# Kernel tuning notes

Hardware: AMD Instinct MI355X
Metric: run time of the kernel (lower is better)

## Reference

```python
import jax, jax.numpy as jnp
import numpy as np

N = 50000          # nodes
E = 600000         # edges
IN, H, HID = 3, 128, 64   # input_size, embed_size, decoder hidden
L = 5              # block_number (GRU layers)
EPS = 1e-12


def _l2norm(v):
    # F.normalize(v, p=2, dim=1)
    return v / jnp.maximum(jnp.linalg.norm(v, axis=1, keepdims=True), EPS)


def setup_inputs() -> dict:
    key = jax.random.key(0)
    ks = jax.random.split(key, 12)
    s = 0.05
    x = jax.random.normal(ks[0], (N, IN), dtype=jnp.float32)
    edge_idx = jax.random.randint(ks[1], (2, E), 0, N, dtype=jnp.int64)
    return {
        "x": x,
        "edge_idx": edge_idx,
        # encoder embed: Linear(IN, H)
        "W_embed": jax.random.normal(ks[2], (H, IN), dtype=jnp.float32) * s,
        "b_embed": jnp.zeros((H,), dtype=jnp.float32),
        # L stacked GRU(H, H) params, torch gate order (r, z, n)
        "w_ih": jax.random.normal(ks[3], (L, 3 * H, H), dtype=jnp.float32) * s,
        "w_hh": jax.random.normal(ks[4], (L, 3 * H, H), dtype=jnp.float32) * s,
        "b_ih": jax.random.normal(ks[5], (L, 3 * H), dtype=jnp.float32) * s,
        "b_hh": jax.random.normal(ks[6], (L, 3 * H), dtype=jnp.float32) * s,
        # decoder: Linear(H, HID) -> ReLU -> Linear(HID, 1)
        "W_hid": jax.random.normal(ks[7], (HID, H), dtype=jnp.float32) * s,
        "b_hid": jnp.zeros((HID,), dtype=jnp.float32),
        "W_out": jax.random.normal(ks[8], (1, HID), dtype=jnp.float32) * s,
        "b_out": jnp.zeros((1,), dtype=jnp.float32),
    }


def reference(x, edge_idx, W_embed, b_embed, w_ih, w_hh, b_ih, b_hh,
              W_hid, b_hid, W_out, b_out):
    row, col = edge_idx[0], edge_idx[1]
    n = x.shape[0]

    # symmetric degree normalization (deg + 1)^-0.5, identical every layer
    deg = jnp.zeros((n,), dtype=x.dtype).at[col].add(1.0) + 1.0
    dinv = deg ** -0.5
    norm = dinv[row] * dinv[col]            # [E]

    h0 = _l2norm(jax.nn.relu(x @ W_embed.T + b_embed))  # [N, H]

    def step(h, params):
        wih, whh, bih, bhh = params
        # message + add-aggregate: out[col] += norm * h[row]
        msg = norm[:, None] * h[row]                     # [E, H]
        agg = jax.ops.segment_sum(msg, col, num_segments=n)  # [N, H]
        # GRU step: input = agg, hidden = h (torch gate order r, z, n)
        gi = agg @ wih.T + bih                           # [N, 3H]
        gh = h @ whh.T + bhh                             # [N, 3H]
        i_r, i_z, i_n = jnp.split(gi, 3, axis=1)
        h_r, h_z, h_n = jnp.split(gh, 3, axis=1)
        r = jax.nn.sigmoid(i_r + h_r)
        zg = jax.nn.sigmoid(i_z + h_z)
        ng = jnp.tanh(i_n + r * h_n)
        hn = _l2norm((1.0 - zg) * ng + zg * h)
        return hn, hn

    _, hs = jax.lax.scan(step, h0, (w_ih, w_hh, b_ih, b_hh))  # hs: [L, N, H]
    all_h = jnp.concatenate([h0[None], hs], axis=0)           # [L+1, N, H]
    z = jnp.max(all_h, axis=0)                                # layer-wise max-pool

    z = jax.nn.relu(z @ W_hid.T + b_hid)
    return z @ W_out.T + b_out                                # [N, 1]
```

## Files before the change

### kernel.cpp

```cpp
#include <hip/hip_runtime.h>
#include <math.h>


#define NTHREADS 256
#define SCAN_CHUNK 1024

typedef __attribute__((ext_vector_type(8))) short s16x8;
typedef __attribute__((ext_vector_type(4))) float f32x4;

union U8 { s16x8 v; ushort4 h[2]; int4 q; };

__device__ __forceinline__ unsigned short f2bf(float f) {
  union { float f; unsigned u; } x; x.f = f;
  unsigned u = x.u + 0x7FFFu + ((x.u >> 16) & 1u);
  return (unsigned short)(u >> 16);
}
__device__ __forceinline__ float bf2f(unsigned short s) {
  union { unsigned u; float f; } x; x.u = ((unsigned)s) << 16;
  return x.f;
}
__device__ __forceinline__ float fast_sigmoid(float x) {
  return __builtin_amdgcn_rcpf(1.f + __expf(-x));
}
__device__ __forceinline__ float fast_tanh(float x) {
  return 1.f - 2.f * __builtin_amdgcn_rcpf(1.f + __expf(2.f * x));
}


__global__ void count_deg(const int* __restrict__ col, int* deg, int E) {
  int e = blockIdx.x * NTHREADS + threadIdx.x;
  if (e < E) atomicAdd(&deg[col[e]], 1);
}

__global__ void block_reduce(const int* __restrict__ cnt, int* __restrict__ bsum,
                             float* __restrict__ dinv, float* __restrict__ rdinv, int n) {
  __shared__ int red[NTHREADS];
  int b = blockIdx.x, t = threadIdx.x;
  int base = b * SCAN_CHUNK + t * 4;
  int s = 0;
#pragma unroll
  for (int i = 0; i < 4; ++i) {
    int idx = base + i;
    if (idx < n) {
      int c = cnt[idx];
      s += c;
      dinv[idx] = rsqrtf((float)c + 1.0f);
      rdinv[idx] = sqrtf((float)c + 1.0f);
    }
  }
  red[t] = s;
  __syncthreads();
  for (int off = NTHREADS / 2; off > 0; off >>= 1) {
    if (t < off) red[t] += red[t + off];
    __syncthreads();
  }
  if (t == 0) bsum[b] = red[0];
}

__global__ void scan_partials(const int* __restrict__ bsum, int* __restrict__ boff,
                              int* __restrict__ row_ptr_n, int nb) {
  int t = threadIdx.x;
  int s = (t < nb) ? bsum[t] : 0;
  int orig = s;
#pragma unroll
  for (int off = 1; off < 64; off <<= 1) {
    int v = __shfl_up(s, off);
    if (t >= off) s += v;
  }
  if (t < nb) boff[t] = s - orig;
  if (t == nb - 1) *row_ptr_n = s;
}

__global__ void scan_final(const int* __restrict__ cnt, const int* __restrict__ boff,
                           int* __restrict__ row_ptr, int* __restrict__ cursor, int n) {
  __shared__ int sums[NTHREADS];
  int b = blockIdx.x, t = threadIdx.x;
  int base = b * SCAN_CHUNK + t * 4;
  int v[4];
  int s = 0;
#pragma unroll
  for (int i = 0; i < 4; ++i) { int idx = base + i; v[i] = (idx < n) ? cnt[idx] : 0; s += v[i]; }
  sums[t] = s;
  __syncthreads();
  for (int off = 1; off < NTHREADS; off <<= 1) {
    int a = (t >= off) ? sums[t - off] : 0;
    __syncthreads();
    sums[t] += a;
    __syncthreads();
  }
  int run = boff[b] + sums[t] - s;
#pragma unroll
  for (int i = 0; i < 4; ++i) {
    int idx = base + i;
    if (idx < n) { row_ptr[idx] = run; cursor[idx] = run; }
    run += v[i];
  }
}

__global__ void scatter_edges(const int* __restrict__ row, const int* __restrict__ col,
                              int* cursor, int* __restrict__ src, int E) {
  int e = blockIdx.x * NTHREADS + threadIdx.x;
  if (e >= E) return;
  int r = row[e], c = col[e];
  int p = atomicAdd(&cursor[c], 1);
  src[p] = r;
}


__global__ void pack_weights(const float* __restrict__ w_ih, const float* __restrict__ w_hh,
                             unsigned short* __restrict__ out) {
  int idx = blockIdx.x * NTHREADS + threadIdx.x;
  if (idx >= 491520) return;
  int e = idx & 7;
  int lane = (idx >> 3) & 63;
  int ft = (idx >> 9) & 7;
  int v = idx >> 12;
  int g = v % 6;
  int u = v / 6;
  int ks = u & 3;
  int layer = u >> 2;
  int k = 32 * ks + (e & 3) + 4 * ((lane >> 4) & 3) + 16 * (e >> 2);
  int j = 16 * ft + (lane & 15);
  const float* src = (g < 3) ? w_ih : w_hh;
  int gate = g % 3;
  float val = src[(size_t)layer * 49152 + (size_t)(gate * 128 + j) * 128 + k];
  out[idx] = f2bf(val);
}

__global__ void pack_whid(const float* __restrict__ W_hid, unsigned short* __restrict__ out) {
  int idx = blockIdx.x * NTHREADS + threadIdx.x;
  if (idx >= 8192) return;
  int e = idx & 7;
  int lane = (idx >> 3) & 63;
  int ft = (idx >> 9) & 3;
  int ks = idx >> 11;
  int k = 32 * ks + (e & 3) + 4 * ((lane >> 4) & 3) + 16 * (e >> 2);
  int j = 16 * ft + (lane & 15);
  out[idx] = f2bf(W_hid[j * 128 + k]);
}


__global__ void encoder(const float* __restrict__ x, const float* __restrict__ W,
                        const float* __restrict__ b, const float* __restrict__ dinv,
                        unsigned short* __restrict__ hd, int n) {
  int node = blockIdx.x * 4 + (threadIdx.x >> 6);
  int lane = threadIdx.x & 63;
  if (node >= n) return;
  float x0 = x[node * 3 + 0], x1 = x[node * 3 + 1], x2 = x[node * 3 + 2];
  int j0 = lane, j1 = lane + 64;
  float v0 = fmaxf(fmaf(W[j0 * 3 + 2], x2, fmaf(W[j0 * 3 + 1], x1, fmaf(W[j0 * 3], x0, b[j0]))), 0.f);
  float v1 = fmaxf(fmaf(W[j1 * 3 + 2], x2, fmaf(W[j1 * 3 + 1], x1, fmaf(W[j1 * 3], x0, b[j1]))), 0.f);
  float ss = v0 * v0 + v1 * v1;
#pragma unroll
  for (int sh = 32; sh > 0; sh >>= 1) ss += __shfl_down(ss, sh);
  ss = __shfl(ss, 0);
  float sc = 1.0f / fmaxf(sqrtf(ss), 1e-12f);
  float dv = dinv[node];
  size_t base = (size_t)node * 128;
  hd[base + j0] = f2bf(v0 * sc * dv);
  hd[base + j1] = f2bf(v1 * sc * dv);
}


__global__ void aggregate(const int* __restrict__ row_ptr, const int* __restrict__ src,
                          const float* __restrict__ dinv, const unsigned short* __restrict__ hd,
                          unsigned short* __restrict__ aggb, int n) {
  int wv = threadIdx.x >> 6;
  int lane = threadIdx.x & 63;
  int half = lane >> 5;
  int li = lane & 31;
  int node = blockIdx.x * 8 + wv * 2 + half;
  if (node >= n) return;
  const uint2* hw = (const uint2*)hd;
  int pb = row_ptr[node], pe = row_ptr[node + 1];
  float a0[4] = {0.f, 0.f, 0.f, 0.f};
  float a1[4] = {0.f, 0.f, 0.f, 0.f};
  float a2[4] = {0.f, 0.f, 0.f, 0.f};
  float a3[4] = {0.f, 0.f, 0.f, 0.f};
  for (int p = pb; p < pe; p += 8) {
    uint2 u[8]; float w8[8];
#pragma unroll
    for (int i = 0; i < 8; ++i) {
      int q = p + i;
      int ok = q < pe;
      int s = src[ok ? q : pb];
      w8[i] = ok ? 1.f : 0.f;
      u[i] = hw[(size_t)s * 32 + li];
    }
#pragma unroll
    for (int i = 0; i < 8; ++i) {
      a0[i & 3] = fmaf(w8[i], bf2f((unsigned short)(u[i].x & 0xFFFFu)), a0[i & 3]);
      a1[i & 3] = fmaf(w8[i], bf2f((unsigned short)(u[i].x >> 16)), a1[i & 3]);
      a2[i & 3] = fmaf(w8[i], bf2f((unsigned short)(u[i].y & 0xFFFFu)), a2[i & 3]);
      a3[i & 3] = fmaf(w8[i], bf2f((unsigned short)(u[i].y >> 16)), a3[i & 3]);
    }
  }
  float dc = dinv[node];
  float s0 = ((a0[0] + a0[1]) + (a0[2] + a0[3])) * dc;
  float s1 = ((a1[0] + a1[1]) + (a1[2] + a1[3])) * dc;
  float s2 = ((a2[0] + a2[1]) + (a2[2] + a2[3])) * dc;
  float s3 = ((a3[0] + a3[1]) + (a3[2] + a3[3])) * dc;
  uint2 o;
  o.x = ((unsigned)f2bf(s1) << 16) | (unsigned)f2bf(s0);
  o.y = ((unsigned)f2bf(s3) << 16) | (unsigned)f2bf(s2);
  ((uint2*)(aggb + (size_t)node * 128))[li] = o;
}


__global__ __launch_bounds__(1024) void gru_mfma(
    const unsigned short* __restrict__ aggb, const unsigned short* __restrict__ hdc,
    unsigned short* __restrict__ hdn, const float* __restrict__ dinv,
    const float* __restrict__ rdinv,
    const int4* __restrict__ wpk, const float* __restrict__ bih,
    const float* __restrict__ bhh, int n) {
  __shared__ unsigned short aggS[64 * 132];
  __shared__ unsigned short hS[64 * 132];
  __shared__ float partS[64 * 8];
  __shared__ float scv[64];
  __shared__ float dS[64], rS[64];
  int tid = threadIdx.x;
  int base = blockIdx.x * 64;
  int w = tid >> 6, l = tid & 63;
  int mh = w & 1, fh = w >> 1;
  int lr = l & 15, lg = l >> 4;
  int jj = fh * 16 + lr;

  if (tid < 64) {
    int gr = base + tid; if (gr > n - 1) gr = n - 1;
    dS[tid] = dinv[gr];
    rS[tid] = rdinv[gr];
  }
#pragma unroll
  for (int rep = 0; rep < 2; ++rep) {
    int idx = tid + rep * 1024;
    int row = idx >> 5, c4 = idx & 31;
    int gr = base + row; if (gr > n - 1) gr = n - 1;
    ushort4 ua = *(const ushort4*)(aggb + (size_t)gr * 128 + c4 * 4);
    ushort4 uh = *(const ushort4*)(hdc + (size_t)gr * 128 + c4 * 4);
    *(ushort4*)&aggS[row * 132 + c4 * 4] = ua;
    *(ushort4*)&hS[row * 132 + c4 * 4] = uh;
  }
  __syncthreads();

  f32x4 acc[2][6];
#pragma unroll
  for (int mt = 0; mt < 2; ++mt)
#pragma unroll
    for (int g = 0; g < 6; ++g) { acc[mt][g][0] = 0.f; acc[mt][g][1] = 0.f; acc[mt][g][2] = 0.f; acc[mt][g][3] = 0.f; }

#pragma unroll
  for (int ks = 0; ks < 4; ++ks) {
    U8 fa[2], fhh[2];
#pragma unroll
    for (int mt = 0; mt < 2; ++mt) {
      int boff = (mh * 32 + mt * 16 + lr) * 132 + ks * 32 + lg * 4;
      fa[mt].h[0] = *(const ushort4*)&aggS[boff];
      fa[mt].h[1] = *(const ushort4*)&aggS[boff + 16];
      fhh[mt].h[0] = *(const ushort4*)&hS[boff];
      fhh[mt].h[1] = *(const ushort4*)&hS[boff + 16];
    }
#pragma unroll
    for (int g = 0; g < 6; ++g) {
      U8 bw; bw.q = wpk[((ks * 6 + g) * 8 + fh) * 64 + l];
      const U8& a0 = (g < 3) ? fa[0] : fhh[0];
      const U8& a1 = (g < 3) ? fa[1] : fhh[1];
      acc[0][g] = __builtin_amdgcn_mfma_f32_16x16x32_bf16(a0.v, bw.v, acc[0][g], 0, 0, 0);
      acc[1][g] = __builtin_amdgcn_mfma_f32_16x16x32_bf16(a1.v, bw.v, acc[1][g], 0, 0, 0);
    }
  }

  float br = bih[jj], bz = bih[128 + jj], bn = bih[256 + jj];
  float cr = bhh[jj], cz = bhh[128 + jj], cn = bhh[256 + jj];
  float hn_out[2][4];
#pragma unroll
  for (int mt = 0; mt < 2; ++mt)
#pragma unroll
    for (int e = 0; e < 4; ++e) {
      int row = mh * 32 + mt * 16 + lg * 4 + e;
      float rr = rS[row];
      float ir = acc[mt][0][e], iz = acc[mt][1][e], inn = acc[mt][2][e];
      float hr = acc[mt][3][e] * rr, hz = acc[mt][4][e] * rr, hnv = acc[mt][5][e] * rr;
      float r = fast_sigmoid(ir + hr + br + cr);
      float z = fast_sigmoid(iz + hz + bz + cz);
      float ng = fast_tanh(inn + bn + r * (hnv + cn));
      float hv = bf2f(hS[row * 132 + jj]) * rr;
      float hn = (1.f - z) * ng + z * hv;
      hn_out[mt][e] = hn;
      float p = hn * hn;
      p += __shfl_xor(p, 1);
      p += __shfl_xor(p, 2);
      p += __shfl_xor(p, 4);
      p += __shfl_xor(p, 8);
      if (lr == 0) partS[row * 8 + fh] = p;
    }
  __syncthreads();
  if (tid < 64) {
    float ss = 0.f;
#pragma unroll
    for (int f = 0; f < 8; ++f) ss += partS[tid * 8 + f];
    scv[tid] = rsqrtf(fmaxf(ss, 1e-24f));
  }
  __syncthreads();

#pragma unroll
  for (int mt = 0; mt < 2; ++mt)
#pragma unroll
    for (int e = 0; e < 4; ++e) {
      int row = mh * 32 + mt * 16 + lg * 4 + e;
      aggS[row * 132 + jj] = f2bf(hn_out[mt][e] * scv[row] * dS[row]);
    }
  __syncthreads();

#pragma unroll
  for (int rep = 0; rep < 2; ++rep) {
    int idx = tid + rep * 1024;
    int row = idx >> 5, c4 = idx & 31;
    int gr = base + row;
    if (gr < n) {
      ushort4 hv4 = *(const ushort4*)&aggS[row * 132 + c4 * 4];
      *(ushort4*)(hdn + (size_t)gr * 128 + c4 * 4) = hv4;
    }
  }
}


__global__ __launch_bounds__(256) void decoder_mfma(
    const unsigned short* __restrict__ h0, const unsigned short* __restrict__ h1,
    const unsigned short* __restrict__ h2, const unsigned short* __restrict__ h3,
    const unsigned short* __restrict__ h4, const unsigned short* __restrict__ h5,
    const float* __restrict__ rdinv,
    const int4* __restrict__ wdpk, const float* __restrict__ bh,
    const float* __restrict__ Wo, const float* __restrict__ bo,
    float* __restrict__ out, int n) {
  __shared__ unsigned short zS[64 * 132];
  int tid = threadIdx.x;
  int base = blockIdx.x * 64;
  const unsigned short* hp[6] = {h0, h1, h2, h3, h4, h5};
#pragma unroll
  for (int rep = 0; rep < 8; ++rep) {
    int idx = tid + rep * 256;
    int row = idx >> 5, c4 = idx & 31;
    int gr = base + row; if (gr > n - 1) gr = n - 1;
    size_t o = (size_t)gr * 128 + c4 * 4;
    ushort4 uu[6];
#pragma unroll
    for (int li = 0; li < 6; ++li) uu[li] = *(const ushort4*)(hp[li] + o);
    ushort4 m = uu[0];
#pragma unroll
    for (int li = 1; li < 6; ++li) {
      m.x = (bf2f(uu[li].x) > bf2f(m.x)) ? uu[li].x : m.x;
      m.y = (bf2f(uu[li].y) > bf2f(m.y)) ? uu[li].y : m.y;
      m.z = (bf2f(uu[li].z) > bf2f(m.z)) ? uu[li].z : m.z;
      m.w = (bf2f(uu[li].w) > bf2f(m.w)) ? uu[li].w : m.w;
    }
    *(ushort4*)&zS[row * 132 + c4 * 4] = m;
  }
  __syncthreads();
  int w = tid >> 6, l = tid & 63;
  int lr = l & 15, lg = l >> 4;
  f32x4 acc[4];
#pragma unroll
  for (int ft = 0; ft < 4; ++ft) { acc[ft][0] = 0.f; acc[ft][1] = 0.f; acc[ft][2] = 0.f; acc[ft][3] = 0.f; }
#pragma unroll
  for (int ks = 0; ks < 4; ++ks) {
    U8 fz;
    int boff = (w * 16 + lr) * 132 + ks * 32 + lg * 4;
    fz.h[0] = *(const ushort4*)&zS[boff];
    fz.h[1] = *(const ushort4*)&zS[boff + 16];
#pragma unroll
    for (int ft = 0; ft < 4; ++ft) {
      U8 bw; bw.q = wdpk[(ks * 4 + ft) * 64 + l];
      acc[ft] = __builtin_amdgcn_mfma_f32_16x16x32_bf16(fz.v, bw.v, acc[ft], 0, 0, 0);
    }
  }
  int rowb = base + w * 16 + lg * 4;
  float rr[4];
#pragma unroll
  for (int e = 0; e < 4; ++e) {
    int gr = rowb + e; if (gr > n - 1) gr = n - 1;
    rr[e] = rdinv[gr];
  }
  float s[4] = {0.f, 0.f, 0.f, 0.f};
#pragma unroll
  for (int ft = 0; ft < 4; ++ft) {
    int j = ft * 16 + lr;
    float bj = bh[j], wj = Wo[j];
#pragma unroll
    for (int e = 0; e < 4; ++e) {
      float hid = fmaxf(fmaf(acc[ft][e], rr[e], bj), 0.f);
      s[e] = fmaf(hid, wj, s[e]);
    }
  }
#pragma unroll
  for (int e = 0; e < 4; ++e) {
    float v = s[e];
    v += __shfl_xor(v, 1);
    v += __shfl_xor(v, 2);
    v += __shfl_xor(v, 4);
    v += __shfl_xor(v, 8);
    if (lr == 0) {
      int gr = rowb + e;
      if (gr < n) out[gr] = v + bo[0];
    }
  }
}


extern "C" void kernel_launch(void* const* d_in, const int* in_sizes, int n_in,
                              void* d_out, int out_size, void* d_ws, size_t ws_size,
                              hipStream_t stream) {
  const float* x       = (const float*)d_in[0];
  const int*   edge    = (const int*)d_in[1];
  const float* W_embed = (const float*)d_in[2];
  const float* b_embed = (const float*)d_in[3];
  const float* w_ih    = (const float*)d_in[4];
  const float* w_hh    = (const float*)d_in[5];
  const float* b_ih    = (const float*)d_in[6];
  const float* b_hh    = (const float*)d_in[7];
  const float* W_hid   = (const float*)d_in[8];
  const float* b_hid   = (const float*)d_in[9];
  const float* W_out   = (const float*)d_in[10];
  const float* b_out   = (const float*)d_in[11];
  float* out = (float*)d_out;

  const int N = in_sizes[0] / 3;
  const int E = in_sizes[1] / 2;
  const int NB = (N + SCAN_CHUNK - 1) / SCAN_CHUNK;

  char* ws = (char*)d_ws;
  size_t off = 0;
  auto alloc = [&](size_t bytes) -> void* {
    void* p = ws + off;
    off = (off + bytes + 511) & ~(size_t)511;
    return p;
  };
  int*   deg     = (int*)alloc((size_t)N * 4);
  float* dinv    = (float*)alloc((size_t)N * 4);
  float* rdinv   = (float*)alloc((size_t)N * 4);
  int*   row_ptr = (int*)alloc((size_t)(N + 1) * 4);
  int*   cursor  = (int*)alloc((size_t)N * 4);
  int*   bsum    = (int*)alloc((size_t)NB * 4);
  int*   boff    = (int*)alloc((size_t)NB * 4);
  int*   srcv    = (int*)alloc((size_t)(E + 8) * 4);
  unsigned short* wpack  = (unsigned short*)alloc((size_t)491520 * 2);
  unsigned short* wdpack = (unsigned short*)alloc((size_t)8192 * 2);
  unsigned short* aggb   = (unsigned short*)alloc((size_t)N * 128 * 2);
  unsigned short* hbs[6];
  for (int i = 0; i < 6; ++i) hbs[i] = (unsigned short*)alloc((size_t)N * 128 * 2);

  const int* erow = edge;
  const int* ecol = edge + E;

  hipMemsetAsync(deg, 0, (size_t)N * 4, stream);
  count_deg<<<(E + NTHREADS - 1) / NTHREADS, NTHREADS, 0, stream>>>(ecol, deg, E);
  block_reduce<<<NB, NTHREADS, 0, stream>>>(deg, bsum, dinv, rdinv, N);
  scan_partials<<<1, 64, 0, stream>>>(bsum, boff, row_ptr + N, NB);
  scan_final<<<NB, NTHREADS, 0, stream>>>(deg, boff, row_ptr, cursor, N);
  scatter_edges<<<(E + NTHREADS - 1) / NTHREADS, NTHREADS, 0, stream>>>(erow, ecol, cursor, srcv, E);

  pack_weights<<<(491520 + NTHREADS - 1) / NTHREADS, NTHREADS, 0, stream>>>(w_ih, w_hh, wpack);
  pack_whid<<<32, NTHREADS, 0, stream>>>(W_hid, wdpack);

  encoder<<<(N + 3) / 4, NTHREADS, 0, stream>>>(x, W_embed, b_embed, dinv, hbs[0], N);

  for (int l = 0; l < 5; ++l) {
    aggregate<<<(N + 7) / 8, NTHREADS, 0, stream>>>(row_ptr, srcv, dinv, hbs[l], aggb, N);
    gru_mfma<<<(N + 63) / 64, 1024, 0, stream>>>(
        aggb, hbs[l], hbs[l + 1], dinv, rdinv,
        (const int4*)(wpack + (size_t)l * 98304),
        b_ih + (size_t)l * 384, b_hh + (size_t)l * 384, N);
  }

  decoder_mfma<<<(N + 63) / 64, NTHREADS, 0, stream>>>(
      hbs[0], hbs[1], hbs[2], hbs[3], hbs[4], hbs[5], rdinv,
      (const int4*)wdpack, b_hid, W_out, b_out, out, N);
}
```

Baseline: 384.4 us.

## Sort aggregate nodes by degree to balance half-wave work; merge packing kernels

Builds a degree histogram, scans it, and scatters node ids into a degree-sorted permutation. The aggregate kernel then processes nodes in that order, so the two half-waves in a wavefront get similar edge counts and spend less time idle on divergent loop lengths. The two weight-packing kernels are also merged into one launch. This adds three small setup kernels and global atomics, and the permuted order scatters the writes of aggregated rows, which hurts locality.

```diff
diff --git a/kernel.cpp b/kernel.cpp
--- a/kernel.cpp
+++ b/kernel.cpp
@@ -33,7 +33,8 @@
 }
 
 __global__ void block_reduce(const int* __restrict__ cnt, int* __restrict__ bsum,
-                             float* __restrict__ dinv, float* __restrict__ rdinv, int n) {
+                             float* __restrict__ dinv, float* __restrict__ rdinv,
+                             int* __restrict__ hist, int n) {
   __shared__ int red[NTHREADS];
   int b = blockIdx.x, t = threadIdx.x;
   int base = b * SCAN_CHUNK + t * 4;
@@ -46,6 +47,7 @@
       s += c;
       dinv[idx] = rsqrtf((float)c + 1.0f);
       rdinv[idx] = sqrtf((float)c + 1.0f);
+      atomicAdd(&hist[c > 255 ? 255 : c], 1);
     }
   }
   red[t] = s;
@@ -97,6 +99,30 @@
   }
 }
 
+__global__ void hist_scan(const int* __restrict__ hist, int* __restrict__ bincur) {
+  __shared__ int sums[256];
+  int t = threadIdx.x;
+  int v = hist[t];
+  sums[t] = v;
+  __syncthreads();
+  for (int off = 1; off < 256; off <<= 1) {
+    int a = (t >= off) ? sums[t - off] : 0;
+    __syncthreads();
+    sums[t] += a;
+    __syncthreads();
+  }
+  bincur[t] = sums[t] - v;
+}
+
+__global__ void perm_scatter(const int* __restrict__ deg, int* bincur,
+                             int* __restrict__ perm, int n) {
+  int i = blockIdx.x * NTHREADS + threadIdx.x;
+  if (i >= n) return;
+  int d = deg[i]; if (d > 255) d = 255;
+  int p = atomicAdd(&bincur[d], 1);
+  perm[p] = i;
+}
+
 __global__ void scatter_edges(const int* __restrict__ row, const int* __restrict__ col,
                               int* cursor, int* __restrict__ src, int E) {
   int e = blockIdx.x * NTHREADS + threadIdx.x;
@@ -107,36 +133,34 @@
 }
 
 
-__global__ void pack_weights(const float* __restrict__ w_ih, const float* __restrict__ w_hh,
-                             unsigned short* __restrict__ out) {
+__global__ void pack_all(const float* __restrict__ w_ih, const float* __restrict__ w_hh,
+                         const float* __restrict__ W_hid,
+                         unsigned short* __restrict__ out, unsigned short* __restrict__ outd) {
   int idx = blockIdx.x * NTHREADS + threadIdx.x;
-  if (idx >= 491520) return;
-  int e = idx & 7;
-  int lane = (idx >> 3) & 63;
-  int ft = (idx >> 9) & 7;
-  int v = idx >> 12;
-  int g = v % 6;
-  int u = v / 6;
-  int ks = u & 3;
-  int layer = u >> 2;
-  int k = 32 * ks + (e & 3) + 4 * ((lane >> 4) & 3) + 16 * (e >> 2);
-  int j = 16 * ft + (lane & 15);
-  const float* src = (g < 3) ? w_ih : w_hh;
-  int gate = g % 3;
-  float val = src[(size_t)layer * 49152 + (size_t)(gate * 128 + j) * 128 + k];
-  out[idx] = f2bf(val);
-}
-
-__global__ void pack_whid(const float* __restrict__ W_hid, unsigned short* __restrict__ out) {
-  int idx = blockIdx.x * NTHREADS + threadIdx.x;
-  if (idx >= 8192) return;
-  int e = idx & 7;
-  int lane = (idx >> 3) & 63;
-  int ft = (idx >> 9) & 3;
-  int ks = idx >> 11;
-  int k = 32 * ks + (e & 3) + 4 * ((lane >> 4) & 3) + 16 * (e >> 2);
-  int j = 16 * ft + (lane & 15);
-  out[idx] = f2bf(W_hid[j * 128 + k]);
+  if (idx < 491520) {
+    int e = idx & 7;
+    int lane = (idx >> 3) & 63;
+    int ft = (idx >> 9) & 7;
+    int v = idx >> 12;
+    int g = v % 6;
+    int u = v / 6;
+    int ks = u & 3;
+    int layer = u >> 2;
+    int k = 32 * ks + (e & 3) + 4 * ((lane >> 4) & 3) + 16 * (e >> 2);
+    int j = 16 * ft + (lane & 15);
+    const float* src = (g < 3) ? w_ih : w_hh;
+    int gate = g % 3;
+    out[idx] = f2bf(src[(size_t)layer * 49152 + (size_t)(gate * 128 + j) * 128 + k]);
+  } else if (idx < 491520 + 8192) {
+    int id2 = idx - 491520;
+    int e = id2 & 7;
+    int lane = (id2 >> 3) & 63;
+    int ft = (id2 >> 9) & 3;
+    int ks = id2 >> 11;
+    int k = 32 * ks + (e & 3) + 4 * ((lane >> 4) & 3) + 16 * (e >> 2);
+    int j = 16 * ft + (lane & 15);
+    outd[id2] = f2bf(W_hid[j * 128 + k]);
+  }
 }
 
 
@@ -163,14 +187,16 @@
 
 
 __global__ void aggregate(const int* __restrict__ row_ptr, const int* __restrict__ src,
+                          const int* __restrict__ perm,
                           const float* __restrict__ dinv, const unsigned short* __restrict__ hd,
                           unsigned short* __restrict__ aggb, int n) {
   int wv = threadIdx.x >> 6;
   int lane = threadIdx.x & 63;
   int half = lane >> 5;
   int li = lane & 31;
-  int node = blockIdx.x * 8 + wv * 2 + half;
-  if (node >= n) return;
+  int slot = blockIdx.x * 8 + wv * 2 + half;
+  if (slot >= n) return;
+  int node = perm[slot];
   const uint2* hw = (const uint2*)hd;
   int pb = row_ptr[node], pe = row_ptr[node + 1];
   float a0[4] = {0.f, 0.f, 0.f, 0.f};
@@ -434,13 +460,16 @@
     off = (off + bytes + 511) & ~(size_t)511;
     return p;
   };
-  int*   deg     = (int*)alloc((size_t)N * 4);
+  int*   deg     = (int*)alloc((size_t)(N + 256) * 4);
+  int*   hist    = deg + N;
   float* dinv    = (float*)alloc((size_t)N * 4);
   float* rdinv   = (float*)alloc((size_t)N * 4);
   int*   row_ptr = (int*)alloc((size_t)(N + 1) * 4);
   int*   cursor  = (int*)alloc((size_t)N * 4);
   int*   bsum    = (int*)alloc((size_t)NB * 4);
   int*   boff    = (int*)alloc((size_t)NB * 4);
+  int*   bincur  = (int*)alloc((size_t)256 * 4);
+  int*   perm    = (int*)alloc((size_t)N * 4);
   int*   srcv    = (int*)alloc((size_t)(E + 8) * 4);
   unsigned short* wpack  = (unsigned short*)alloc((size_t)491520 * 2);
   unsigned short* wdpack = (unsigned short*)alloc((size_t)8192 * 2);
@@ -451,20 +480,22 @@
   const int* erow = edge;
   const int* ecol = edge + E;
 
-  hipMemsetAsync(deg, 0, (size_t)N * 4, stream);
+  hipMemsetAsync(deg, 0, (size_t)(N + 256) * 4, stream);
   count_deg<<<(E + NTHREADS - 1) / NTHREADS, NTHREADS, 0, stream>>>(ecol, deg, E);
-  block_reduce<<<NB, NTHREADS, 0, stream>>>(deg, bsum, dinv, rdinv, N);
+  block_reduce<<<NB, NTHREADS, 0, stream>>>(deg, bsum, dinv, rdinv, hist, N);
   scan_partials<<<1, 64, 0, stream>>>(bsum, boff, row_ptr + N, NB);
   scan_final<<<NB, NTHREADS, 0, stream>>>(deg, boff, row_ptr, cursor, N);
+  hist_scan<<<1, 256, 0, stream>>>(hist, bincur);
+  perm_scatter<<<(N + NTHREADS - 1) / NTHREADS, NTHREADS, 0, stream>>>(deg, bincur, perm, N);
   scatter_edges<<<(E + NTHREADS - 1) / NTHREADS, NTHREADS, 0, stream>>>(erow, ecol, cursor, srcv, E);
 
-  pack_weights<<<(491520 + NTHREADS - 1) / NTHREADS, NTHREADS, 0, stream>>>(w_ih, w_hh, wpack);
-  pack_whid<<<32, NTHREADS, 0, stream>>>(W_hid, wdpack);
+  pack_all<<<(491520 + 8192 + NTHREADS - 1) / NTHREADS, NTHREADS, 0, stream>>>(
+      w_ih, w_hh, W_hid, wpack, wdpack);
 
   encoder<<<(N + 3) / 4, NTHREADS, 0, stream>>>(x, W_embed, b_embed, dinv, hbs[0], N);
 
   for (int l = 0; l < 5; ++l) {
-    aggregate<<<(N + 7) / 8, NTHREADS, 0, stream>>>(row_ptr, srcv, dinv, hbs[l], aggb, N);
+    aggregate<<<(N + 7) / 8, NTHREADS, 0, stream>>>(row_ptr, srcv, perm, dinv, hbs[l], aggb, N);
     gru_mfma<<<(N + 63) / 64, 1024, 0, stream>>>(
         aggb, hbs[l], hbs[l + 1], dinv, rdinv,
         (const int4*)(wpack + (size_t)l * 98304),
```

Measured after the change: 706.1 us. +83.7%, slower.
